# Kernel optimization log

Hardware: AMD Instinct MI355X
Metric: run time of the kernel (lower is better)

Reference implementation:

```python
import math
import jax, jax.numpy as jnp
from jax import lax
import numpy as np

BLEND_RATIO = 0.15


def _cosine_window(h, w, br):
    # numpy: static shapes, matches torch _cosine_window
    yh = max(1, int(round(h * br)))
    xw = max(1, int(round(w * br)))
    y = np.ones((h, 1), dtype=np.float64)
    ty = np.linspace(0.0, math.pi, yh)
    fy = 0.5 * (1.0 - np.cos(ty))
    y[:yh, 0] = fy
    y[-yh:, 0] = fy[::-1]
    x = np.ones((1, w), dtype=np.float64)
    tx = np.linspace(0.0, math.pi, xw)
    fx = 0.5 * (1.0 - np.cos(tx))
    x[0, :xw] = fx
    x[0, -xw:] = fx[::-1]
    return np.clip(y @ x, 1e-6, 1.0)


def setup_inputs() -> dict:
    key = jax.random.key(0)
    k1, k2 = jax.random.split(key)
    x = jax.random.normal(k1, (8, 3, 1024, 1024), dtype=jnp.float32)
    kernels = jax.random.uniform(k2, (4, 4, 15, 15), dtype=jnp.float32)
    return {"x": x, "kernels": kernels}


def reference(x, kernels):
    b, c, H, W = x.shape
    ny, nx, K, _ = kernels.shape
    pad = K // 2
    hh = [H // ny + (1 if y < H % ny else 0) for y in range(ny)]
    ww = [W // nx + (1 if i < W % nx else 0) for i in range(nx)]
    y0 = [0]
    for h in hh[:-1]:
        y0.append(y0[-1] + h)
    x0 = [0]
    for w in ww[:-1]:
        x0.append(x0[-1] + w)

    out = jnp.zeros_like(x)
    acc = jnp.zeros((b, 1, H, W), dtype=x.dtype)
    for j in range(ny):
        for i in range(nx):
            h, w = hh[j], ww[i]
            ys, xs = y0[j], x0[i]
            k = kernels[j, i]
            k = k / (k.sum() + 1e-12)
            # depthwise weight (c, 1, K, K)
            wgt = jnp.broadcast_to(k[None, None], (c, 1, K, K))
            patch = lax.dynamic_slice(x, (0, 0, ys, xs), (b, c, h, w))
            padded = jnp.pad(patch, ((0, 0), (0, 0), (pad, pad), (pad, pad)), mode="edge")
            y_hat = lax.conv_general_dilated(
                padded, wgt, window_strides=(1, 1), padding="VALID",
                dimension_numbers=("NCHW", "OIHW", "NCHW"), feature_group_count=c)
            wmask = jnp.asarray(_cosine_window(h, w, BLEND_RATIO), dtype=x.dtype)  # (h, w)
            out = out.at[:, :, ys:ys + h, xs:xs + w].add(y_hat * wmask[None, None])
            acc = acc.at[:, :, ys:ys + h, xs:xs + w].add(
                jnp.broadcast_to(wmask[None, None], (b, 1, h, w)))
    return out / jnp.clip(acc, 1e-6, None)
```

## Files before the change

kernel.cpp:

```cpp
#include <hip/hip_runtime.h>

#define HH    1024
#define WW    1024
#define KS    15
#define PAD   7
#define CELL  256
#define BX    64
#define TROWS 142
#define TCOLS 80
#define NITER 16
#define CHN   18
#define AWS_CELL_BYTES (KS * 1024)

typedef _Float16     f16x8 __attribute__((ext_vector_type(8)));
typedef _Float16     f16x4 __attribute__((ext_vector_type(4)));
typedef float        f32x4 __attribute__((ext_vector_type(4)));
typedef unsigned int u32x4 __attribute__((ext_vector_type(4)));

static __device__ __forceinline__ void light_barrier() {
    asm volatile("s_waitcnt lgkmcnt(0)\n\ts_barrier" ::: "memory");
}

__global__ __launch_bounds__(256) void pb_prep_kernel(
    const float* __restrict__ kern, unsigned int* __restrict__ aws)
{
    const int cell = blockIdx.x;
    const int tid  = threadIdx.x;
    const int lane = tid & 63;
    const float* kp = kern + cell * (KS * KS);

    float s = 0.f;
    #pragma unroll
    for (int i = 0; i < 4; ++i) {
        int t = lane + 64 * i;
        s += (t < KS * KS) ? kp[t] : 0.f;
    }
    #pragma unroll
    for (int m = 1; m < 64; m <<= 1) s += __shfl_xor(s, m, 64);
    const float inv = 1.0f / (s + 1e-12f);

    const int i  = tid >> 4;
    const int k2 = tid & 15;
    unsigned int* wp = aws + cell * (AWS_CELL_BYTES / 4) + tid;

    for (int dy = 0; dy < KS; ++dy) {
        float v0 = 0.f, v1 = 0.f;
        int dx0 = 2 * k2 - i - 1;
        int dx1 = dx0 + 1;
        if (dx0 >= 0 && dx0 < KS) v0 = kp[dy * KS + dx0] * inv;
        if (dx1 >= 0 && dx1 < KS) v1 = kp[dy * KS + dx1] * inv;
        f16x4 h; h[0] = (_Float16)v0; h[1] = (_Float16)v1; h[2] = 0; h[3] = 0;
        unsigned long long u = __builtin_bit_cast(unsigned long long, h);
        wp[dy * 256] = (unsigned int)u;
    }
}

__global__ __launch_bounds__(256, 4) void pb_mfma_kernel(
    const float* __restrict__ x,
    const unsigned int* __restrict__ aws,
    float* __restrict__ out)
{
    __shared__ __align__(16) _Float16 s_tile[TROWS * TCOLS];

    const int tid  = threadIdx.x;
    const int lane = tid & 63;
    const int w    = tid >> 6;
    const int g    = lane >> 4;
    const int cc   = lane & 15;

    const int bx0 = blockIdx.x * BX;
    const int ci  = blockIdx.x >> 2;
    const int cj  = blockIdx.y;
    const int bc  = blockIdx.z;

    const int cellx0 = ci * CELL;
    const int celly0 = cj * CELL, celly1 = celly0 + CELL - 1;

    const float* plane = x + (size_t)bc * HH * WW;

    const u32x4* ap = (const u32x4*)(aws + (cj * 4 + ci) * (AWS_CELL_BYTES / 4))
                      + cc * 4 + g;
    u32x4 af[KS];
    #pragma unroll
    for (int dy = 0; dy < KS; ++dy) af[dy] = ap[dy * 64];
    #pragma unroll
    for (int dy = 0; dy < KS; ++dy) asm volatile("" : "+v"(af[dy]));

    auto stage_addr = [&](int strip, int lc, int idx) -> const float* {
        int r20  = idx / 20;
        int c4   = idx - r20 * 20;
        int row  = lc * 16 + r20;
        int gy   = min(max(celly0 + strip * 128 - PAD + row, celly0), celly1);
        int gx0  = bx0 - 8 + 4 * c4;
        int gx0c = min(max(gx0, cellx0), cellx0 + CELL - 4);
        return plane + (size_t)gy * WW + gx0c;
    };
    auto write_group = [&](int lc, int idx, float4 v) {
        int r20 = idx / 20;
        int c4  = idx - r20 * 20;
        int row = lc * 16 + r20;
        int gx0 = bx0 - 8 + 4 * c4;
        bool lo = gx0 <  cellx0;
        bool hi = gx0 >  cellx0 + CELL - 4;
        float e0 = hi ? v.w : v.x;
        float e1 = lo ? v.x : (hi ? v.w : v.y);
        float e2 = lo ? v.x : (hi ? v.w : v.z);
        float e3 = lo ? v.x : v.w;
        f16x4 h;
        h[0] = (_Float16)e0; h[1] = (_Float16)e1;
        h[2] = (_Float16)e2; h[3] = (_Float16)e3;
        *(f16x4*)(s_tile + row * TCOLS + 4 * c4) = h;
    };
    auto issue_chunk = [&](int gch, float4& v0, float4& v1, bool& h1) {
        int strip = gch >= 9;
        int lc    = gch - 9 * strip;
        int ng    = (lc == 8) ? 280 : 320;
        v0 = *(const float4*)stage_addr(strip, lc, tid);
        h1 = 256 + tid < ng;
        if (h1) v1 = *(const float4*)stage_addr(strip, lc, 256 + tid);
    };
    auto write_chunk = [&](int gch, float4 v0, float4 v1, bool h1) {
        int strip = gch >= 9;
        int lc    = gch - 9 * strip;
        (void)strip;
        write_group(lc, tid, v0);
        if (h1) write_group(lc, 256 + tid, v1);
    };

    {
        float4 a0, a1, b0, b1, c0, c1; bool ha1, hb1, hc1;
        issue_chunk(0, a0, a1, ha1);
        issue_chunk(1, b0, b1, hb1);
        issue_chunk(2, c0, c1, hc1);
        write_chunk(0, a0, a1, ha1);
        write_chunk(1, b0, b1, hb1);
        write_chunk(2, c0, c1, hc1);
    }
    float4 pA0, pA1, pB0, pB1; bool hA1, hB1;
    issue_chunk(3, pA0, pA1, hA1);
    issue_chunk(4, pB0, pB1, hB1);
    light_barrier();

    const _Float16* bbase = s_tile + cc * TCOLS + w * 16 + g * 8;
    float* oplane = out + (size_t)bc * HH * WW;

    #pragma unroll
    for (int t = 0; t < NITER; ++t) {
        const int strip = t >> 3;
        const int jpl   = t & 7;

        float4 n0 = {0,0,0,0}, n1 = {0,0,0,0}; bool hn1 = false;
        if (t + 5 < CHN) issue_chunk(t + 5, n0, n1, hn1);

        f32x4 acc0 = {0.f, 0.f, 0.f, 0.f};
        f32x4 acc1 = {0.f, 0.f, 0.f, 0.f};
        #pragma unroll
        for (int dy = 0; dy < KS; ++dy) {
            f16x8 b = *(const f16x8*)(bbase + (16 * jpl + dy) * TCOLS);
            if (dy & 1)
                acc1 = __builtin_amdgcn_mfma_f32_16x16x32_f16(
                           __builtin_bit_cast(f16x8, af[dy]), b, acc1, 0, 0, 0);
            else
                acc0 = __builtin_amdgcn_mfma_f32_16x16x32_f16(
                           __builtin_bit_cast(f16x8, af[dy]), b, acc0, 0, 0, 0);
        }
        f32x4 r = acc0 + acc1;
        float* op = oplane
                  + (size_t)(celly0 + strip * 128 + 16 * jpl + cc) * WW
                  + bx0 + 16 * w + 4 * g;
        *(f32x4*)op = r;

        if (t + 3 < CHN) write_chunk(t + 3, pA0, pA1, hA1);
        light_barrier();

        pA0 = pB0; pA1 = pB1; hA1 = hB1;
        pB0 = n0;  pB1 = n1;  hB1 = hn1;
    }
}

extern "C" void kernel_launch(void* const* d_in, const int* in_sizes, int n_in,
                              void* d_out, int out_size, void* d_ws, size_t ws_size,
                              hipStream_t stream) {
    (void)in_sizes; (void)n_in; (void)ws_size; (void)out_size;
    const float* x    = (const float*)d_in[0];
    const float* kern = (const float*)d_in[1];
    float* out        = (float*)d_out;
    unsigned int* aws = (unsigned int*)d_ws;

    pb_prep_kernel<<<16, 256, 0, stream>>>(kern, aws);
    dim3 grid(WW / BX, 4, 8 * 3);
    pb_mfma_kernel<<<grid, 256, 0, stream>>>(x, aws, out);
}
```

Baseline: 56.00 us.

## Process two row tiles per iteration with 32-row staging chunks

Restructures the main loop so each iteration computes two 16-row output tiles (two independent MFMA chains sharing the weight fragment), halving the number of barriers. Staging chunks grow from 16 to 32 rows and are scheduled by static issue/write tables with a 4-slot register ring. The occupancy hint drops from 4 to 3 blocks per SIMD to make room for the larger in-flight register buffers. This trades fewer synchronizations and more MFMA ILP for higher register pressure and lower occupancy.

```diff
diff --git a/kernel.cpp b/kernel.cpp
--- a/kernel.cpp
+++ b/kernel.cpp
@@ -8,8 +8,8 @@
 #define BX    64
 #define TROWS 142
 #define TCOLS 80
-#define NITER 16
-#define CHN   18
+#define NSUP  8
+#define CHN   10
 #define AWS_CELL_BYTES (KS * 1024)
 
 typedef _Float16     f16x8 __attribute__((ext_vector_type(8)));
@@ -55,7 +55,7 @@
     }
 }
 
-__global__ __launch_bounds__(256, 4) void pb_mfma_kernel(
+__global__ __launch_bounds__(256, 3) void pb_mfma_kernel(
     const float* __restrict__ x,
     const unsigned int* __restrict__ aws,
     float* __restrict__ out)
@@ -89,7 +89,7 @@
     auto stage_addr = [&](int strip, int lc, int idx) -> const float* {
         int r20  = idx / 20;
         int c4   = idx - r20 * 20;
-        int row  = lc * 16 + r20;
+        int row  = lc * 32 + r20;
         int gy   = min(max(celly0 + strip * 128 - PAD + row, celly0), celly1);
         int gx0  = bx0 - 8 + 4 * c4;
         int gx0c = min(max(gx0, cellx0), cellx0 + CELL - 4);
@@ -98,7 +98,7 @@
     auto write_group = [&](int lc, int idx, float4 v) {
         int r20 = idx / 20;
         int c4  = idx - r20 * 20;
-        int row = lc * 16 + r20;
+        int row = lc * 32 + r20;
         int gx0 = bx0 - 8 + 4 * c4;
         bool lo = gx0 <  cellx0;
         bool hi = gx0 >  cellx0 + CELL - 4;
@@ -111,70 +111,84 @@
         h[2] = (_Float16)e2; h[3] = (_Float16)e3;
         *(f16x4*)(s_tile + row * TCOLS + 4 * c4) = h;
     };
-    auto issue_chunk = [&](int gch, float4& v0, float4& v1, bool& h1) {
-        int strip = gch >= 9;
-        int lc    = gch - 9 * strip;
-        int ng    = (lc == 8) ? 280 : 320;
-        v0 = *(const float4*)stage_addr(strip, lc, tid);
-        h1 = 256 + tid < ng;
-        if (h1) v1 = *(const float4*)stage_addr(strip, lc, 256 + tid);
-    };
-    auto write_chunk = [&](int gch, float4 v0, float4 v1, bool h1) {
-        int strip = gch >= 9;
-        int lc    = gch - 9 * strip;
+
+    float4 pa[4], pb[4], pc[4];
+    bool   h1[4], h2[4];
+
+    auto issue_chunk = [&](int c) {
+        int strip = c >= 5;
+        int lc    = c - 5 * strip;
+        int ng    = (lc == 4) ? 280 : 640;
+        int s     = c & 3;
+        pa[s] = *(const float4*)stage_addr(strip, lc, tid);
+        h1[s] = 256 + tid < ng;
+        h2[s] = 512 + tid < ng;
+        if (h1[s]) pb[s] = *(const float4*)stage_addr(strip, lc, 256 + tid);
+        if (h2[s]) pc[s] = *(const float4*)stage_addr(strip, lc, 512 + tid);
+    };
+    auto write_chunk = [&](int c) {
+        int strip = c >= 5;
+        int lc    = c - 5 * strip;
+        int s     = c & 3;
         (void)strip;
-        write_group(lc, tid, v0);
-        if (h1) write_group(lc, 256 + tid, v1);
-    };
-
-    {
-        float4 a0, a1, b0, b1, c0, c1; bool ha1, hb1, hc1;
-        issue_chunk(0, a0, a1, ha1);
-        issue_chunk(1, b0, b1, hb1);
-        issue_chunk(2, c0, c1, hc1);
-        write_chunk(0, a0, a1, ha1);
-        write_chunk(1, b0, b1, hb1);
-        write_chunk(2, c0, c1, hc1);
-    }
-    float4 pA0, pA1, pB0, pB1; bool hA1, hB1;
-    issue_chunk(3, pA0, pA1, hA1);
-    issue_chunk(4, pB0, pB1, hB1);
+        write_group(lc, tid, pa[s]);
+        if (h1[s]) write_group(lc, 256 + tid, pb[s]);
+        if (h2[s]) write_group(lc, 512 + tid, pc[s]);
+    };
+
+    issue_chunk(0); write_chunk(0);
+    issue_chunk(1); write_chunk(1);
+    issue_chunk(2);
+    issue_chunk(3);
     light_barrier();
+
+    static constexpr int ISS[NSUP][2] = {{4,-1},{5,-1},{6,7},{8,-1},{9,-1},{-1,-1},{-1,-1},{-1,-1}};
+    static constexpr int WRT[NSUP][2] = {{2,-1},{3,-1},{4,-1},{5,6},{7,-1},{8,-1},{9,-1},{-1,-1}};
 
     const _Float16* bbase = s_tile + cc * TCOLS + w * 16 + g * 8;
     float* oplane = out + (size_t)bc * HH * WW;
 
     #pragma unroll
-    for (int t = 0; t < NITER; ++t) {
-        const int strip = t >> 3;
-        const int jpl   = t & 7;
-
-        float4 n0 = {0,0,0,0}, n1 = {0,0,0,0}; bool hn1 = false;
-        if (t + 5 < CHN) issue_chunk(t + 5, n0, n1, hn1);
-
-        f32x4 acc0 = {0.f, 0.f, 0.f, 0.f};
-        f32x4 acc1 = {0.f, 0.f, 0.f, 0.f};
+    for (int t = 0; t < NSUP; ++t) {
+        const int strip = t >> 2;
+        const int tl    = t & 3;
+        const int jpl0  = 2 * tl;
+        const int jpl1  = 2 * tl + 1;
+
+        if (ISS[t][0] >= 0) issue_chunk(ISS[t][0]);
+        if (ISS[t][1] >= 0) issue_chunk(ISS[t][1]);
+
+        f32x4 a00 = {0,0,0,0}, a01 = {0,0,0,0};
+        f32x4 a10 = {0,0,0,0}, a11 = {0,0,0,0};
         #pragma unroll
         for (int dy = 0; dy < KS; ++dy) {
-            f16x8 b = *(const f16x8*)(bbase + (16 * jpl + dy) * TCOLS);
-            if (dy & 1)
-                acc1 = __builtin_amdgcn_mfma_f32_16x16x32_f16(
-                           __builtin_bit_cast(f16x8, af[dy]), b, acc1, 0, 0, 0);
-            else
-                acc0 = __builtin_amdgcn_mfma_f32_16x16x32_f16(
-                           __builtin_bit_cast(f16x8, af[dy]), b, acc0, 0, 0, 0);
+            f16x8 b0 = *(const f16x8*)(bbase + (16 * jpl0 + dy) * TCOLS);
+            f16x8 b1 = *(const f16x8*)(bbase + (16 * jpl1 + dy) * TCOLS);
+            f16x8 a  = __builtin_bit_cast(f16x8, af[dy]);
+            if (dy & 1) {
+                a01 = __builtin_amdgcn_mfma_f32_16x16x32_f16(a, b0, a01, 0, 0, 0);
+                a11 = __builtin_amdgcn_mfma_f32_16x16x32_f16(a, b1, a11, 0, 0, 0);
+            } else {
+                a00 = __builtin_amdgcn_mfma_f32_16x16x32_f16(a, b0, a00, 0, 0, 0);
+                a10 = __builtin_amdgcn_mfma_f32_16x16x32_f16(a, b1, a10, 0, 0, 0);
+            }
         }
-        f32x4 r = acc0 + acc1;
-        float* op = oplane
-                  + (size_t)(celly0 + strip * 128 + 16 * jpl + cc) * WW
-                  + bx0 + 16 * w + 4 * g;
-        *(f32x4*)op = r;
-
-        if (t + 3 < CHN) write_chunk(t + 3, pA0, pA1, hA1);
+        f32x4 r0 = a00 + a01;
+        f32x4 r1 = a10 + a11;
+        {
+            float* op0 = oplane
+                + (size_t)(celly0 + strip * 128 + 16 * jpl0 + cc) * WW
+                + bx0 + 16 * w + 4 * g;
+            float* op1 = oplane
+                + (size_t)(celly0 + strip * 128 + 16 * jpl1 + cc) * WW
+                + bx0 + 16 * w + 4 * g;
+            *(f32x4*)op0 = r0;
+            *(f32x4*)op1 = r1;
+        }
+
+        if (WRT[t][0] >= 0) write_chunk(WRT[t][0]);
+        if (WRT[t][1] >= 0) write_chunk(WRT[t][1]);
         light_barrier();
-
-        pA0 = pB0; pA1 = pB1; hA1 = hB1;
-        pB0 = n0;  pB1 = n1;  hB1 = hn1;
     }
 }
 
```

Measured after the change: 56.87 us. No clear change (+1.5%).

## Replace per-tap LDS reads with DPP row rotation and deepen staging pipeline

Applied to the files above, without the earlier changes.

Each iteration now loads only two 16-row fragments from LDS and builds the 15 shifted B operands with DPP row-rotate and lane selects, where it used to do one LDS load per kernel tap. Next-iteration fragments are prefetched, and the staging pipeline is one chunk deeper. Launch bounds drop to 3 waves/SIMD to make room for the extra registers. This trades LDS bandwidth and latency for VALU DPP/select work and lower occupancy. There is also a correctness risk in the rotation and select logic and in the refill-before-barrier ordering.

```diff
diff --git a/kernel.cpp b/kernel.cpp
--- a/kernel.cpp
+++ b/kernel.cpp
@@ -21,6 +21,15 @@
     asm volatile("s_waitcnt lgkmcnt(0)\n\ts_barrier" ::: "memory");
 }
 
+static __device__ __forceinline__ u32x4 ror1(u32x4 v) {
+    u32x4 r;
+    #pragma unroll
+    for (int d = 0; d < 4; ++d)
+        r[d] = (unsigned)__builtin_amdgcn_update_dpp(
+                   0, (int)v[d], 0x12F, 0xF, 0xF, false);
+    return r;
+}
+
 __global__ __launch_bounds__(256) void pb_prep_kernel(
     const float* __restrict__ kern, unsigned int* __restrict__ aws)
 {
@@ -55,7 +64,7 @@
     }
 }
 
-__global__ __launch_bounds__(256, 4) void pb_mfma_kernel(
+__global__ __launch_bounds__(256, 3) void pb_mfma_kernel(
     const float* __restrict__ x,
     const unsigned int* __restrict__ aws,
     float* __restrict__ out)
@@ -111,37 +120,41 @@
         h[2] = (_Float16)e2; h[3] = (_Float16)e3;
         *(f16x4*)(s_tile + row * TCOLS + 4 * c4) = h;
     };
-    auto issue_chunk = [&](int gch, float4& v0, float4& v1, bool& h1) {
-        int strip = gch >= 9;
-        int lc    = gch - 9 * strip;
+    auto issue_chunk = [&](int c, float4& v0, float4& v1, bool& h1) {
+        int strip = c >= 9;
+        int lc    = c - 9 * strip;
         int ng    = (lc == 8) ? 280 : 320;
         v0 = *(const float4*)stage_addr(strip, lc, tid);
         h1 = 256 + tid < ng;
         if (h1) v1 = *(const float4*)stage_addr(strip, lc, 256 + tid);
     };
-    auto write_chunk = [&](int gch, float4 v0, float4 v1, bool h1) {
-        int strip = gch >= 9;
-        int lc    = gch - 9 * strip;
+    auto write_chunk = [&](int c, float4 v0, float4 v1, bool h1) {
+        int strip = c >= 9;
+        int lc    = c - 9 * strip;
         (void)strip;
         write_group(lc, tid, v0);
         if (h1) write_group(lc, 256 + tid, v1);
     };
 
     {
-        float4 a0, a1, b0, b1, c0, c1; bool ha1, hb1, hc1;
-        issue_chunk(0, a0, a1, ha1);
-        issue_chunk(1, b0, b1, hb1);
-        issue_chunk(2, c0, c1, hc1);
-        write_chunk(0, a0, a1, ha1);
-        write_chunk(1, b0, b1, hb1);
-        write_chunk(2, c0, c1, hc1);
+        float4 a0, a1, b0, b1, c0, c1, d0, d1; bool ha, hb, hc, hd;
+        issue_chunk(0, a0, a1, ha);
+        issue_chunk(1, b0, b1, hb);
+        issue_chunk(2, c0, c1, hc);
+        issue_chunk(3, d0, d1, hd);
+        write_chunk(0, a0, a1, ha);
+        write_chunk(1, b0, b1, hb);
+        write_chunk(2, c0, c1, hc);
+        write_chunk(3, d0, d1, hd);
     }
     float4 pA0, pA1, pB0, pB1; bool hA1, hB1;
-    issue_chunk(3, pA0, pA1, hA1);
-    issue_chunk(4, pB0, pB1, hB1);
+    issue_chunk(4, pA0, pA1, hA1);
+    issue_chunk(5, pB0, pB1, hB1);
     light_barrier();
 
     const _Float16* bbase = s_tile + cc * TCOLS + w * 16 + g * 8;
+    u32x4 F0 = *(const u32x4*)(bbase);
+    u32x4 F1 = *(const u32x4*)(bbase + 16 * TCOLS);
     float* oplane = out + (size_t)bc * HH * WW;
 
     #pragma unroll
@@ -150,19 +163,42 @@
         const int jpl   = t & 7;
 
         float4 n0 = {0,0,0,0}, n1 = {0,0,0,0}; bool hn1 = false;
-        if (t + 5 < CHN) issue_chunk(t + 5, n0, n1, hn1);
+        if (t + 6 < CHN) issue_chunk(t + 6, n0, n1, hn1);
+
+        u32x4 F0n = F0, F1n = F1;
+        if (t + 1 < NITER) {
+            const int jn = (t + 1) & 7;
+            F0n = *(const u32x4*)(bbase + (16 * jn) * TCOLS);
+            if (jn == 7) {
+                int r1 = min(128 + cc, TROWS - 1);
+                F1n = *(const u32x4*)(s_tile + r1 * TCOLS + w * 16 + g * 8);
+            } else {
+                F1n = *(const u32x4*)(bbase + (16 * jn + 16) * TCOLS);
+            }
+        }
 
         f32x4 acc0 = {0.f, 0.f, 0.f, 0.f};
         f32x4 acc1 = {0.f, 0.f, 0.f, 0.f};
+        u32x4 F0r = F0, F1r = F1;
+        acc0 = __builtin_amdgcn_mfma_f32_16x16x32_f16(
+                   __builtin_bit_cast(f16x8, af[0]),
+                   __builtin_bit_cast(f16x8, F0r), acc0, 0, 0, 0);
         #pragma unroll
-        for (int dy = 0; dy < KS; ++dy) {
-            f16x8 b = *(const f16x8*)(bbase + (16 * jpl + dy) * TCOLS);
+        for (int dy = 1; dy < KS; ++dy) {
+            F0r = ror1(F0r);
+            F1r = ror1(F1r);
+            u32x4 bb;
+            #pragma unroll
+            for (int d = 0; d < 4; ++d)
+                bb[d] = (cc + dy >= 16) ? F1r[d] : F0r[d];
             if (dy & 1)
                 acc1 = __builtin_amdgcn_mfma_f32_16x16x32_f16(
-                           __builtin_bit_cast(f16x8, af[dy]), b, acc1, 0, 0, 0);
+                           __builtin_bit_cast(f16x8, af[dy]),
+                           __builtin_bit_cast(f16x8, bb), acc1, 0, 0, 0);
             else
                 acc0 = __builtin_amdgcn_mfma_f32_16x16x32_f16(
-                           __builtin_bit_cast(f16x8, af[dy]), b, acc0, 0, 0, 0);
+                           __builtin_bit_cast(f16x8, af[dy]),
+                           __builtin_bit_cast(f16x8, bb), acc0, 0, 0, 0);
         }
         f32x4 r = acc0 + acc1;
         float* op = oplane
@@ -170,11 +206,12 @@
                   + bx0 + 16 * w + 4 * g;
         *(f32x4*)op = r;
 
-        if (t + 3 < CHN) write_chunk(t + 3, pA0, pA1, hA1);
+        if (t + 4 < CHN) write_chunk(t + 4, pA0, pA1, hA1);
         light_barrier();
 
         pA0 = pB0; pA1 = pB1; hA1 = hB1;
         pB0 = n0;  pB1 = n1;  hB1 = hn1;
+        F0 = F0n; F1 = F1n;
     }
 }
 
```

Result: slower. 72.96 us (+30.3%).
